# Performance work log

Measured on AMD Instinct MI355X. Metric: run time of the kernel, lower is better.

## Reference

```python
import jax, jax.numpy as jnp
import numpy as np

I, H, L, O = 11, 33, 3, 18

def lstm_layer(x_tbi, W_ih, W_hh, b_ih, b_hh):
    # x_tbi: [T, B, in]; W_ih: [4H, in]; W_hh: [4H, H]
    T, B = x_tbi.shape[0], x_tbi.shape[1]
    # precompute input contribution for all timesteps (one big GEMM)
    xg = jnp.einsum('tbi,gi->tbg', x_tbi, W_ih) + b_ih + b_hh  # [T, B, 4H]
    h0 = jnp.zeros((B, H), x_tbi.dtype)
    c0 = jnp.zeros((B, H), x_tbi.dtype)

    def step(carry, xg_t):
        h, c = carry
        gates = xg_t + h @ W_hh.T                      # [B, 4H]
        i, f, g, o = jnp.split(gates, 4, axis=-1)      # PyTorch gate order i,f,g,o
        i = jax.nn.sigmoid(i)
        f = jax.nn.sigmoid(f)
        g = jnp.tanh(g)
        o = jax.nn.sigmoid(o)
        c = f * c + i * g
        h = o * jnp.tanh(c)
        return (h, c), h

    (hT, cT), ys = jax.lax.scan(step, (h0, c0), xg)
    return ys, hT, cT  # ys: [T, B, H]


def setup_inputs() -> dict:
    key = jax.random.key(0)
    ks = jax.random.split(key, 20)
    B, T = 512, 2048
    s = 1.0 / np.sqrt(H)
    d = {'x': jax.random.normal(ks[0], (B, T, I), jnp.float32)}
    in_sizes = [I, H, H]
    for l in range(L):
        d[f'W_ih{l}'] = jax.random.uniform(ks[1 + 4 * l], (4 * H, in_sizes[l]), jnp.float32, -s, s)
        d[f'W_hh{l}'] = jax.random.uniform(ks[2 + 4 * l], (4 * H, H), jnp.float32, -s, s)
        d[f'b_ih{l}'] = jax.random.uniform(ks[3 + 4 * l], (4 * H,), jnp.float32, -s, s)
        d[f'b_hh{l}'] = jax.random.uniform(ks[4 + 4 * l], (4 * H,), jnp.float32, -s, s)
    d['W1'] = jax.random.normal(ks[13], (4 * O, H), jnp.float32) * 0.05
    d['b1'] = jnp.zeros((4 * O,), jnp.float32)
    d['W2'] = jax.random.normal(ks[14], (O, 4 * O), jnp.float32) * 0.05
    d['b2'] = jnp.zeros((O,), jnp.float32)
    return d


def reference(x, W_ih0, W_hh0, b_ih0, b_hh0, W_ih1, W_hh1, b_ih1, b_hh1,
              W_ih2, W_hh2, b_ih2, b_hh2, W1, b1, W2, b2):
    # x: [B, T, I] (batch_first) -> time-major for scan
    xt = jnp.transpose(x, (1, 0, 2))  # [T, B, I]
    params = [(W_ih0, W_hh0, b_ih0, b_hh0),
              (W_ih1, W_hh1, b_ih1, b_hh1),
              (W_ih2, W_hh2, b_ih2, b_hh2)]
    hiddens = []
    cur = xt
    for (Wi, Wh, bi, bh) in params:
        cur, hT, _ = lstm_layer(cur, Wi, Wh, bi, bh)
        hiddens.append(hT)
    hidden = jnp.stack(hiddens, axis=0)  # [L, B, H] (final hidden state per layer)
    # MLP head (dropout inactive at inference); torch nn.GELU default = exact erf
    h1 = jax.nn.gelu(hidden @ W1.T + b1, approximate=False)
    out = h1 @ W2.T + b2  # [L, B, O]
    return out, hidden
```

## Files before the change

kernel.cpp:

```cpp
#include <hip/hip_runtime.h>
#include <math.h>

#define TT 2048
#define BB 512
#define II 11
#define HH 33
#define NL 3
#define OO 18
#define HSLOT 48

typedef _Float16 h2 __attribute__((ext_vector_type(2)));
typedef _Float16 h8 __attribute__((ext_vector_type(8)));

__device__ __forceinline__ float sigm_f(float x) {
    float e = __expf(-x);
    return __builtin_amdgcn_rcpf(1.0f + e);
}
__device__ __forceinline__ float tanh_f(float x) {
    float e = __expf(2.0f * x);
    return 1.0f - 2.0f * __builtin_amdgcn_rcpf(e + 1.0f);
}

__device__ __forceinline__ float dppx1(float v) {
    return __int_as_float(__builtin_amdgcn_update_dpp(
        0, __float_as_int(v), 0xB1 , 0xF, 0xF, true));
}

__device__ __forceinline__ h8 gldh8(const float* p, int k0, int rem) {
    h8 v;
    #pragma unroll
    for (int i = 0; i < 8; ++i) v[i] = (_Float16)((k0 + i < rem) ? p[k0 + i] : 0.0f);
    return v;
}
__device__ __forceinline__ h2 gldh2(const float* p, int k0, int rem) {
    h2 v;
    v.x = (_Float16)((k0 + 0 < rem) ? p[k0 + 0] : 0.0f);
    v.y = (_Float16)((k0 + 1 < rem) ? p[k0 + 1] : 0.0f);
    return v;
}

#define FD(a, p, q) a = __builtin_amdgcn_fdot2((p), (q), a, false)
#define DQ(v, W0, W1, W2, W3) do { \
    FD(a0, (v).s01, (W0).s01); FD(a1, (v).s01, (W1).s01); FD(a2, (v).s01, (W2).s01); FD(a3, (v).s01, (W3).s01); \
    FD(a0, (v).s23, (W0).s23); FD(a1, (v).s23, (W1).s23); FD(a2, (v).s23, (W2).s23); FD(a3, (v).s23, (W3).s23); \
    FD(a0, (v).s45, (W0).s45); FD(a1, (v).s45, (W1).s45); FD(a2, (v).s45, (W2).s45); FD(a3, (v).s45, (W3).s45); \
    FD(a0, (v).s67, (W0).s67); FD(a1, (v).s67, (W1).s67); FD(a2, (v).s67, (W2).s67); FD(a3, (v).s67, (W3).s67); \
} while (0)
#define D1Q(v) do { \
    FD(a0, (v), wi0t); FD(a1, (v), wi1t); FD(a2, (v), wi2t); FD(a3, (v), wi3t); \
} while (0)
#define D1QH(v) do { \
    FD(a0, (v), wh0t); FD(a1, (v), wh1t); FD(a2, (v), wh2t); FD(a3, (v), wh3t); \
} while (0)

__global__ __launch_bounds__(256, 2) void lstm_pipeline_kernel(
    const float* __restrict__ x,
    const float* __restrict__ Wih0, const float* __restrict__ Whh0,
    const float* __restrict__ bih0, const float* __restrict__ bhh0,
    const float* __restrict__ Wih1, const float* __restrict__ Whh1,
    const float* __restrict__ bih1, const float* __restrict__ bhh1,
    const float* __restrict__ Wih2, const float* __restrict__ Whh2,
    const float* __restrict__ bih2, const float* __restrict__ bhh2,
    const float* __restrict__ W1, const float* __restrict__ b1,
    const float* __restrict__ W2, const float* __restrict__ b2,
    float* __restrict__ hidden_out,
    float* __restrict__ outp)
{
    __shared__ __align__(16) _Float16 buf[2][NL + 1][HSLOT];
    __shared__ float hfin[NL][HH + 1];
    __shared__ float h1s[NL][4 * OO];

    const int tid = threadIdx.x;
    const int bg  = blockIdx.x;

    for (int i = tid; i < 2 * (NL + 1) * HSLOT; i += 256)
        ((_Float16*)buf)[i] = (_Float16)0.0f;

    const bool comp = (tid < 2 * 99);
    const int  u    = tid >> 1;
    const int  hf   = tid & 1;
    const int  l    = (u < 33) ? 0 : (u < 66) ? 1 : 2;
    const int  j    = u - 33 * l;
    const int  koff = hf ? 16 : 0;

    const int  pi   = tid - 200;
    const bool pref = (pi >= 0) && (pi < II);
    const int  pic  = pref ? pi : 0;
    const float* xrow = x + (size_t)bg * TT * II + pic;

    h8 z8 = {0,0,0,0,0,0,0,0};
    h2 z2 = {(_Float16)0.0f, (_Float16)0.0f};
    h8 wi00=z8,wi01=z8, wi10=z8,wi11=z8, wi20=z8,wi21=z8, wi30=z8,wi31=z8;
    h2 wi0t=z2, wi1t=z2, wi2t=z2, wi3t=z2;
    h8 wh00=z8,wh01=z8, wh10=z8,wh11=z8, wh20=z8,wh21=z8, wh30=z8,wh31=z8;
    h2 wh0t=z2, wh1t=z2, wh2t=z2, wh3t=z2;
    float b0 = 0.0f, b1v = 0.0f, b2v = 0.0f, b3v = 0.0f;

    if (comp) {
        if (!hf) {
            const float* bip = (l == 0) ? bih0 : (l == 1) ? bih1 : bih2;
            const float* bhp = (l == 0) ? bhh0 : (l == 1) ? bhh1 : bhh2;
            b0  = bip[0 * HH + j] + bhp[0 * HH + j];
            b1v = bip[1 * HH + j] + bhp[1 * HH + j];
            b2v = bip[2 * HH + j] + bhp[2 * HH + j];
            b3v = bip[3 * HH + j] + bhp[3 * HH + j];
        }
        const float* Wi = (l == 0) ? Wih0 : (l == 1) ? Wih1 : Wih2;
        const float* Wh = (l == 0) ? Whh0 : (l == 1) ? Whh1 : Whh2;
        const int kin = (l == 0) ? II : HH;
        const float* r0 = Wi + (0 * HH + j) * kin;
        const float* r1 = Wi + (1 * HH + j) * kin;
        const float* r2 = Wi + (2 * HH + j) * kin;
        const float* r3 = Wi + (3 * HH + j) * kin;
        wi00 = gldh8(r0, koff, kin); wi01 = gldh8(r0, koff + 8, kin);
        wi10 = gldh8(r1, koff, kin); wi11 = gldh8(r1, koff + 8, kin);
        wi20 = gldh8(r2, koff, kin); wi21 = gldh8(r2, koff + 8, kin);
        wi30 = gldh8(r3, koff, kin); wi31 = gldh8(r3, koff + 8, kin);
        if (hf) {
            wi0t = gldh2(r0, 32, kin); wi1t = gldh2(r1, 32, kin);
            wi2t = gldh2(r2, 32, kin); wi3t = gldh2(r3, 32, kin);
        }
        const float* s0p = Wh + (0 * HH + j) * HH;
        const float* s1p = Wh + (1 * HH + j) * HH;
        const float* s2p = Wh + (2 * HH + j) * HH;
        const float* s3p = Wh + (3 * HH + j) * HH;
        wh00 = gldh8(s0p, koff, HH); wh01 = gldh8(s0p, koff + 8, HH);
        wh10 = gldh8(s1p, koff, HH); wh11 = gldh8(s1p, koff + 8, HH);
        wh20 = gldh8(s2p, koff, HH); wh21 = gldh8(s2p, koff + 8, HH);
        wh30 = gldh8(s3p, koff, HH); wh31 = gldh8(s3p, koff + 8, HH);
        if (hf) {
            wh0t = gldh2(s0p, 32, HH); wh1t = gldh2(s1p, 32, HH);
            wh2t = gldh2(s2p, 32, HH); wh3t = gldh2(s3p, 32, HH);
        }
    }

    const float kX = hf ? 2.0f : -1.0f;
    const float AX = hf ? 1.0f : 0.0f;
    const float BX = hf ? -2.0f : 1.0f;

    __syncthreads();
    float v_next = 0.0f, v_next2 = 0.0f;
    if (pref) {
        buf[0][0][pi] = (_Float16)xrow[0];
        v_next  = xrow[II];
        v_next2 = xrow[2 * II];
    }
    __syncthreads();

    float c = 0.0f;

    const _Float16* rin[2]  = { &buf[0][l][0],     &buf[1][l][0] };
    const _Float16* rown[2] = { &buf[0][l + 1][0], &buf[1][l + 1][0] };
    _Float16*       wrp[2]  = { &buf[0][l + 1][j], &buf[1][l + 1][j] };
    _Float16*       pxp[2]  = { &buf[0][0][pic],   &buf[1][0][pic] };

    auto step = [&](int s, int rp, bool check, bool out, bool xload, bool xstore)
        __attribute__((always_inline)) {
        const int wp = rp ^ 1;
        if (pref) {
            if (xstore) *pxp[wp] = (_Float16)v_next;
            v_next = v_next2;
            if (xload) v_next2 = xrow[(size_t)(s + 3) * II];
        }
        const bool active = check ? (comp && (s >= l) && (s - l < TT)) : comp;
        if (active) {
            const _Float16* ri = rin[rp];
            const _Float16* ro = rown[rp];
            const h8 vi0 = *(const h8*)(ri + koff);
            const h8 vi1 = *(const h8*)(ri + koff + 8);
            const h2 vit = *(const h2*)(ri + 32);
            const h8 vo0 = *(const h8*)(ro + koff);
            const h8 vo1 = *(const h8*)(ro + koff + 8);
            const h2 vot = *(const h2*)(ro + 32);

            float a0 = b0, a1 = b1v, a2 = b2v, a3 = b3v;
            DQ(vi0, wi00, wi10, wi20, wi30);
            DQ(vi1, wi01, wi11, wi21, wi31);
            DQ(vo0, wh00, wh10, wh20, wh30);
            DQ(vo1, wh01, wh11, wh21, wh31);
            D1Q(vit);
            D1QH(vot);

            a0 += dppx1(a0); a1 += dppx1(a1);
            a2 += dppx1(a2); a3 += dppx1(a3);

            const float aXv = hf ? a2 : a0;
            const float eX  = __expf(kX * aXv);
            const float rX  = __builtin_amdgcn_rcpf(1.0f + eX);
            const float xg  = __builtin_fmaf(BX, rX, AX);
            const float yg  = sigm_f(hf ? a3 : a1);

            const float xp = dppx1(xg);
            const float yp = dppx1(yg);
            const float ig = hf ? xp : xg;
            const float fg = hf ? yp : yg;
            const float gg = hf ? xg : xp;
            const float og = hf ? yg : yp;

            c = __builtin_fmaf(fg, c, ig * gg);
            const float hnew = og * tanh_f(c);

            if (!hf) {
                *wrp[wp] = (_Float16)hnew;
                if (out && (s - l == TT - 1)) {
                    hidden_out[((size_t)l * BB + bg) * HH + j] = hnew;
                    hfin[l][j] = hnew;
                }
            }
        }
        __syncthreads();
    };

    step(0, 0, true, false, true, true);
    step(1, 1, true, false, true, true);
    for (int s = 2; s < TT - 4; s += 2) {
        step(s,     0, false, false, true, true);
        step(s + 1, 1, false, false, true, true);
    }
    step(TT - 4, 0, false, false, true,  true);
    step(TT - 3, 1, false, false, false, true);
    step(TT - 2, 0, false, false, false, true);
    step(TT - 1, 1, false, true,  false, false);
    step(TT,     0, true,  true,  false, false);
    step(TT + 1, 1, true,  true,  false, false);

    if (tid < 4 * OO) {
        #pragma unroll
        for (int ml = 0; ml < NL; ++ml) {
            float a = b1[tid];
            #pragma unroll
            for (int k = 0; k < HH; ++k) a += hfin[ml][k] * W1[tid * HH + k];
            h1s[ml][tid] = 0.5f * a * (1.0f + erff(a * 0.70710678118654752f));
        }
    }
    __syncthreads();
    if (tid < NL * OO) {
        const int ol = tid / OO, o = tid % OO;
        float a = b2[o];
        #pragma unroll
        for (int m = 0; m < 4 * OO; ++m) a += h1s[ol][m] * W2[o * (4 * OO) + m];
        outp[((size_t)ol * BB + bg) * OO + o] = a;
    }
}

extern "C" void kernel_launch(void* const* d_in, const int* in_sizes, int n_in,
                              void* d_out, int out_size, void* d_ws, size_t ws_size,
                              hipStream_t stream) {
    const float* x    = (const float*)d_in[0];
    const float* Wih0 = (const float*)d_in[1];
    const float* Whh0 = (const float*)d_in[2];
    const float* bih0 = (const float*)d_in[3];
    const float* bhh0 = (const float*)d_in[4];
    const float* Wih1 = (const float*)d_in[5];
    const float* Whh1 = (const float*)d_in[6];
    const float* bih1 = (const float*)d_in[7];
    const float* bhh1 = (const float*)d_in[8];
    const float* Wih2 = (const float*)d_in[9];
    const float* Whh2 = (const float*)d_in[10];
    const float* bih2 = (const float*)d_in[11];
    const float* bhh2 = (const float*)d_in[12];
    const float* W1   = (const float*)d_in[13];
    const float* b1   = (const float*)d_in[14];
    const float* W2   = (const float*)d_in[15];
    const float* b2   = (const float*)d_in[16];

    float* out    = (float*)d_out;
    float* hidden = out + NL * BB * OO;

    lstm_pipeline_kernel<<<BB, 256, 0, stream>>>(
        x, Wih0, Whh0, bih0, bhh0, Wih1, Whh1, bih1, bhh1,
        Wih2, Whh2, bih2, bhh2, W1, b1, W2, b2, hidden, out);
}
```

Measured before the change: 1.094 ms.

## Switch recurrent dot products from fp16 fdot2 to packed fp32 FMA

Replaces the half-precision weights, the shared hidden-state buffers and the fdot2 accumulation with fp32 storage and v_pk_fma_f32 packed FMAs over float2 pairs. Each thread now keeps 72 float2 weight registers, so the launch bounds drop to one block per SIMD group. The change removes fp16 conversions and improves accuracy, but it doubles register and LDS footprint, adds more FMA instructions per step, and lowers occupancy.

```diff
diff --git a/kernel.cpp b/kernel.cpp
--- a/kernel.cpp
+++ b/kernel.cpp
@@ -7,10 +7,9 @@
 #define HH 33
 #define NL 3
 #define OO 18
-#define HSLOT 48
-
-typedef _Float16 h2 __attribute__((ext_vector_type(2)));
-typedef _Float16 h8 __attribute__((ext_vector_type(8)));
+#define FSLOT 40
+
+typedef float f2 __attribute__((ext_vector_type(2)));
 
 __device__ __forceinline__ float sigm_f(float x) {
     float e = __expf(-x);
@@ -26,34 +25,9 @@
         0, __float_as_int(v), 0xB1 , 0xF, 0xF, true));
 }
 
-__device__ __forceinline__ h8 gldh8(const float* p, int k0, int rem) {
-    h8 v;
-    #pragma unroll
-    for (int i = 0; i < 8; ++i) v[i] = (_Float16)((k0 + i < rem) ? p[k0 + i] : 0.0f);
-    return v;
-}
-__device__ __forceinline__ h2 gldh2(const float* p, int k0, int rem) {
-    h2 v;
-    v.x = (_Float16)((k0 + 0 < rem) ? p[k0 + 0] : 0.0f);
-    v.y = (_Float16)((k0 + 1 < rem) ? p[k0 + 1] : 0.0f);
-    return v;
-}
-
-#define FD(a, p, q) a = __builtin_amdgcn_fdot2((p), (q), a, false)
-#define DQ(v, W0, W1, W2, W3) do { \
-    FD(a0, (v).s01, (W0).s01); FD(a1, (v).s01, (W1).s01); FD(a2, (v).s01, (W2).s01); FD(a3, (v).s01, (W3).s01); \
-    FD(a0, (v).s23, (W0).s23); FD(a1, (v).s23, (W1).s23); FD(a2, (v).s23, (W2).s23); FD(a3, (v).s23, (W3).s23); \
-    FD(a0, (v).s45, (W0).s45); FD(a1, (v).s45, (W1).s45); FD(a2, (v).s45, (W2).s45); FD(a3, (v).s45, (W3).s45); \
-    FD(a0, (v).s67, (W0).s67); FD(a1, (v).s67, (W1).s67); FD(a2, (v).s67, (W2).s67); FD(a3, (v).s67, (W3).s67); \
-} while (0)
-#define D1Q(v) do { \
-    FD(a0, (v), wi0t); FD(a1, (v), wi1t); FD(a2, (v), wi2t); FD(a3, (v), wi3t); \
-} while (0)
-#define D1QH(v) do { \
-    FD(a0, (v), wh0t); FD(a1, (v), wh1t); FD(a2, (v), wh2t); FD(a3, (v), wh3t); \
-} while (0)
-
-__global__ __launch_bounds__(256, 2) void lstm_pipeline_kernel(
+#define PK(acc, w, v) asm("v_pk_fma_f32 %0, %1, %2, %0" : "+v"(acc) : "v"(w), "v"(v))
+
+__global__ __launch_bounds__(256, 1) void lstm_pipeline_kernel(
     const float* __restrict__ x,
     const float* __restrict__ Wih0, const float* __restrict__ Whh0,
     const float* __restrict__ bih0, const float* __restrict__ bhh0,
@@ -66,15 +40,15 @@
     float* __restrict__ hidden_out,
     float* __restrict__ outp)
 {
-    __shared__ __align__(16) _Float16 buf[2][NL + 1][HSLOT];
+    __shared__ __align__(16) float buf[2][NL + 1][FSLOT];
     __shared__ float hfin[NL][HH + 1];
     __shared__ float h1s[NL][4 * OO];
 
     const int tid = threadIdx.x;
     const int bg  = blockIdx.x;
 
-    for (int i = tid; i < 2 * (NL + 1) * HSLOT; i += 256)
-        ((_Float16*)buf)[i] = (_Float16)0.0f;
+    for (int i = tid; i < 2 * (NL + 1) * FSLOT; i += 256)
+        ((float*)buf)[i] = 0.0f;
 
     const bool comp = (tid < 2 * 99);
     const int  u    = tid >> 1;
@@ -88,12 +62,12 @@
     const int  pic  = pref ? pi : 0;
     const float* xrow = x + (size_t)bg * TT * II + pic;
 
-    h8 z8 = {0,0,0,0,0,0,0,0};
-    h2 z2 = {(_Float16)0.0f, (_Float16)0.0f};
-    h8 wi00=z8,wi01=z8, wi10=z8,wi11=z8, wi20=z8,wi21=z8, wi30=z8,wi31=z8;
-    h2 wi0t=z2, wi1t=z2, wi2t=z2, wi3t=z2;
-    h8 wh00=z8,wh01=z8, wh10=z8,wh11=z8, wh20=z8,wh21=z8, wh30=z8,wh31=z8;
-    h2 wh0t=z2, wh1t=z2, wh2t=z2, wh3t=z2;
+    f2 wI[4][9], wH[4][9];
+    #pragma unroll
+    for (int g = 0; g < 4; ++g) {
+        #pragma unroll
+        for (int r = 0; r < 9; ++r) { wI[g][r] = (f2){0.f, 0.f}; wH[g][r] = (f2){0.f, 0.f}; }
+    }
     float b0 = 0.0f, b1v = 0.0f, b2v = 0.0f, b3v = 0.0f;
 
     if (comp) {
@@ -108,29 +82,19 @@
         const float* Wi = (l == 0) ? Wih0 : (l == 1) ? Wih1 : Wih2;
         const float* Wh = (l == 0) ? Whh0 : (l == 1) ? Whh1 : Whh2;
         const int kin = (l == 0) ? II : HH;
-        const float* r0 = Wi + (0 * HH + j) * kin;
-        const float* r1 = Wi + (1 * HH + j) * kin;
-        const float* r2 = Wi + (2 * HH + j) * kin;
-        const float* r3 = Wi + (3 * HH + j) * kin;
-        wi00 = gldh8(r0, koff, kin); wi01 = gldh8(r0, koff + 8, kin);
-        wi10 = gldh8(r1, koff, kin); wi11 = gldh8(r1, koff + 8, kin);
-        wi20 = gldh8(r2, koff, kin); wi21 = gldh8(r2, koff + 8, kin);
-        wi30 = gldh8(r3, koff, kin); wi31 = gldh8(r3, koff + 8, kin);
-        if (hf) {
-            wi0t = gldh2(r0, 32, kin); wi1t = gldh2(r1, 32, kin);
-            wi2t = gldh2(r2, 32, kin); wi3t = gldh2(r3, 32, kin);
-        }
-        const float* s0p = Wh + (0 * HH + j) * HH;
-        const float* s1p = Wh + (1 * HH + j) * HH;
-        const float* s2p = Wh + (2 * HH + j) * HH;
-        const float* s3p = Wh + (3 * HH + j) * HH;
-        wh00 = gldh8(s0p, koff, HH); wh01 = gldh8(s0p, koff + 8, HH);
-        wh10 = gldh8(s1p, koff, HH); wh11 = gldh8(s1p, koff + 8, HH);
-        wh20 = gldh8(s2p, koff, HH); wh21 = gldh8(s2p, koff + 8, HH);
-        wh30 = gldh8(s3p, koff, HH); wh31 = gldh8(s3p, koff + 8, HH);
-        if (hf) {
-            wh0t = gldh2(s0p, 32, HH); wh1t = gldh2(s1p, 32, HH);
-            wh2t = gldh2(s2p, 32, HH); wh3t = gldh2(s3p, 32, HH);
+        #pragma unroll
+        for (int g = 0; g < 4; ++g) {
+            const float* rw = Wi + (g * HH + j) * kin;
+            const float* rh = Wh + (g * HH + j) * HH;
+            #pragma unroll
+            for (int r = 0; r < 9; ++r) {
+                const int  k    = koff + 2 * r;
+                const bool dead = (!hf) && (r == 8);
+                wI[g][r].x = (!dead && k     < kin) ? rw[k]     : 0.0f;
+                wI[g][r].y = (!dead && k + 1 < kin) ? rw[k + 1] : 0.0f;
+                wH[g][r].x = (!dead && k     < HH)  ? rh[k]     : 0.0f;
+                wH[g][r].y = (!dead && k + 1 < HH)  ? rh[k + 1] : 0.0f;
+            }
         }
     }
 
@@ -141,7 +105,7 @@
     __syncthreads();
     float v_next = 0.0f, v_next2 = 0.0f;
     if (pref) {
-        buf[0][0][pi] = (_Float16)xrow[0];
+        buf[0][0][pi] = xrow[0];
         v_next  = xrow[II];
         v_next2 = xrow[2 * II];
     }
@@ -149,46 +113,52 @@
 
     float c = 0.0f;
 
-    const _Float16* rin[2]  = { &buf[0][l][0],     &buf[1][l][0] };
-    const _Float16* rown[2] = { &buf[0][l + 1][0], &buf[1][l + 1][0] };
-    _Float16*       wrp[2]  = { &buf[0][l + 1][j], &buf[1][l + 1][j] };
-    _Float16*       pxp[2]  = { &buf[0][0][pic],   &buf[1][0][pic] };
+    const float* rin[2]  = { &buf[0][l][0],     &buf[1][l][0] };
+    const float* rown[2] = { &buf[0][l + 1][0], &buf[1][l + 1][0] };
+    float*       wrp[2]  = { &buf[0][l + 1][j], &buf[1][l + 1][j] };
+    float*       pxp[2]  = { &buf[0][0][pic],   &buf[1][0][pic] };
 
     auto step = [&](int s, int rp, bool check, bool out, bool xload, bool xstore)
         __attribute__((always_inline)) {
         const int wp = rp ^ 1;
         if (pref) {
-            if (xstore) *pxp[wp] = (_Float16)v_next;
+            if (xstore) *pxp[wp] = v_next;
             v_next = v_next2;
             if (xload) v_next2 = xrow[(size_t)(s + 3) * II];
         }
         const bool active = check ? (comp && (s >= l) && (s - l < TT)) : comp;
         if (active) {
-            const _Float16* ri = rin[rp];
-            const _Float16* ro = rown[rp];
-            const h8 vi0 = *(const h8*)(ri + koff);
-            const h8 vi1 = *(const h8*)(ri + koff + 8);
-            const h2 vit = *(const h2*)(ri + 32);
-            const h8 vo0 = *(const h8*)(ro + koff);
-            const h8 vo1 = *(const h8*)(ro + koff + 8);
-            const h2 vot = *(const h2*)(ro + 32);
-
-            float a0 = b0, a1 = b1v, a2 = b2v, a3 = b3v;
-            DQ(vi0, wi00, wi10, wi20, wi30);
-            DQ(vi1, wi01, wi11, wi21, wi31);
-            DQ(vo0, wh00, wh10, wh20, wh30);
-            DQ(vo1, wh01, wh11, wh21, wh31);
-            D1Q(vit);
-            D1QH(vot);
-
-            a0 += dppx1(a0); a1 += dppx1(a1);
-            a2 += dppx1(a2); a3 += dppx1(a3);
-
-            const float aXv = hf ? a2 : a0;
+            const float* ri = rin[rp];
+            const float* ro = rown[rp];
+            f2 vi[9], vo[9];
+            #pragma unroll
+            for (int r = 0; r < 9; ++r) {
+                vi[r] = *(const f2*)(ri + koff + 2 * r);
+                vo[r] = *(const f2*)(ro + koff + 2 * r);
+            }
+
+            f2 a0 = {b0, 0.0f}, a1 = {b1v, 0.0f}, a2 = {b2v, 0.0f}, a3 = {b3v, 0.0f};
+            #pragma unroll
+            for (int r = 0; r < 9; ++r) {
+                PK(a0, wI[0][r], vi[r]); PK(a1, wI[1][r], vi[r]);
+                PK(a2, wI[2][r], vi[r]); PK(a3, wI[3][r], vi[r]);
+            }
+            #pragma unroll
+            for (int r = 0; r < 9; ++r) {
+                PK(a0, wH[0][r], vo[r]); PK(a1, wH[1][r], vo[r]);
+                PK(a2, wH[2][r], vo[r]); PK(a3, wH[3][r], vo[r]);
+            }
+
+            float s0 = a0.x + a0.y, s1 = a1.x + a1.y;
+            float s2 = a2.x + a2.y, s3 = a3.x + a3.y;
+            s0 += dppx1(s0); s1 += dppx1(s1);
+            s2 += dppx1(s2); s3 += dppx1(s3);
+
+            const float aXv = hf ? s2 : s0;
             const float eX  = __expf(kX * aXv);
             const float rX  = __builtin_amdgcn_rcpf(1.0f + eX);
             const float xg  = __builtin_fmaf(BX, rX, AX);
-            const float yg  = sigm_f(hf ? a3 : a1);
+            const float yg  = sigm_f(hf ? s3 : s1);
 
             const float xp = dppx1(xg);
             const float yp = dppx1(yg);
@@ -201,7 +171,7 @@
             const float hnew = og * tanh_f(c);
 
             if (!hf) {
-                *wrp[wp] = (_Float16)hnew;
+                *wrp[wp] = hnew;
                 if (out && (s - l == TT - 1)) {
                     hidden_out[((size_t)l * BB + bg) * HH + j] = hnew;
                     hfin[l][j] = hnew;
```

New measurement: 1.244 ms. +13.7%, slower.
